# Kernel optimization log

Measured on AMD Instinct MI355X. Metric: run time of the kernel, lower is better.

Reference implementation:

```python
import jax, jax.numpy as jnp
import numpy as np

B, S, V, E, H, NL, DFF = 16, 16, 64, 64, 8, 4, 2048
L = S * V
DH = E // H
NUM_GRIDS = 100
POI_DIM = 8
OV_DIM = 8


def setup_inputs() -> dict:
    key = jax.random.key(0)
    ks = jax.random.split(key, 32)
    sc = 0.05
    inp = {}
    inp['features'] = jax.random.normal(ks[0], (B, S, V, 3), jnp.float32)
    inp['overlap_tag'] = jax.random.randint(ks[1], (B, S, V), 0, 3)
    inp['poi_id'] = jax.random.randint(ks[2], (B, S, V), 0, NUM_GRIDS + 1)
    # embedders
    inp['W_raw'] = jax.random.normal(ks[3], (3, E), jnp.float32) * sc
    inp['b_raw'] = jnp.zeros((E,), jnp.float32)
    inp['pos_tab'] = jax.random.normal(ks[4], (S, E), jnp.float32) * sc
    inp['type_tab'] = jax.random.normal(ks[5], (V, E), jnp.float32) * sc
    inp['poi_tab'] = jax.random.normal(ks[6], (NUM_GRIDS + 1, POI_DIM), jnp.float32) * sc
    inp['overlap_tab'] = jax.random.normal(ks[7], (3, OV_DIM), jnp.float32) * sc
    inp['W_comb'] = jax.random.normal(ks[8], (E + OV_DIM + POI_DIM, E), jnp.float32) * sc
    inp['b_comb'] = jnp.zeros((E,), jnp.float32)
    # transformer layers (stacked over NL)
    inp['Wqkv'] = jax.random.normal(ks[9], (NL, E, 3 * E), jnp.float32) * sc
    inp['bqkv'] = jnp.zeros((NL, 3 * E), jnp.float32)
    inp['Wo'] = jax.random.normal(ks[10], (NL, E, E), jnp.float32) * sc
    inp['bo'] = jnp.zeros((NL, E), jnp.float32)
    inp['ln1_s'] = jnp.ones((NL, E), jnp.float32)
    inp['ln1_b'] = jnp.zeros((NL, E), jnp.float32)
    inp['W1'] = jax.random.normal(ks[11], (NL, E, DFF), jnp.float32) * sc
    inp['b1'] = jnp.zeros((NL, DFF), jnp.float32)
    inp['W2'] = jax.random.normal(ks[12], (NL, DFF, E), jnp.float32) * sc
    inp['b2'] = jnp.zeros((NL, E), jnp.float32)
    inp['ln2_s'] = jnp.ones((NL, E), jnp.float32)
    inp['ln2_b'] = jnp.zeros((NL, E), jnp.float32)
    inp['W_head'] = jax.random.normal(ks[13], (E, 3), jnp.float32) * sc
    inp['b_head'] = jnp.zeros((3,), jnp.float32)
    return inp


def _layer_norm(x, s, b):
    m = x.mean(-1, keepdims=True)
    v = ((x - m) ** 2).mean(-1, keepdims=True)
    return (x - m) / jnp.sqrt(v + 1e-5) * s + b


def _forward(features, overlap_tag, poi_id, W_raw, b_raw, pos_tab, type_tab,
             poi_tab, overlap_tab, W_comb, b_comb, Wqkv, bqkv, Wo, bo,
             ln1_s, ln1_b, W1, b1, W2, b2, ln2_s, ln2_b, W_head, b_head):
    # padding_idx=0 rows are zero (as in nn.Embedding(padding_idx=0))
    poi_tab = poi_tab.at[0].set(0.0)
    overlap_tab = overlap_tab.at[0].set(0.0)

    zero_mask = (features.sum(-1) == 0).reshape(B, L)  # [B, L]
    ov_idx = jnp.maximum(overlap_tag, 0)
    poi_idx = jnp.maximum(poi_id, 0)

    feat_e = features @ W_raw + b_raw                    # [B,S,V,E]
    concat = jnp.concatenate([feat_e, overlap_tab[ov_idx], poi_tab[poi_idx]], axis=-1)
    x = (concat @ W_comb + b_comb).reshape(B, L, E)      # [B,L,E]

    t_idx = jnp.repeat(jnp.arange(S), V)                 # [L]
    v_idx = jnp.tile(jnp.arange(V), S)                   # [L]
    struct_mask = (t_idx[:, None] != t_idx[None, :]) & (v_idx[:, None] != v_idx[None, :])
    full_mask = struct_mask[None] | zero_mask[:, None, :] | zero_mask[:, :, None]  # [B,L,L]
    bias = jnp.where(full_mask, -jnp.inf, 0.0)[:, None, :, :]  # [B,1,L,L]

    x = x + pos_tab[t_idx][None] + type_tab[v_idx][None]

    scale = 1.0 / jnp.sqrt(jnp.asarray(DH, x.dtype))
    for l in range(NL):
        qkv = x @ Wqkv[l] + bqkv[l]                      # [B,L,3E]
        q, k, v = jnp.split(qkv, 3, axis=-1)
        q = q.reshape(B, L, H, DH)
        k = k.reshape(B, L, H, DH)
        v = v.reshape(B, L, H, DH)
        scores = jnp.einsum('bqhd,bkhd->bhqk', q, k) * scale + bias
        attn = jax.nn.softmax(scores, axis=-1)
        o = jnp.einsum('bhqk,bkhd->bqhd', attn, v).reshape(B, L, E)
        x = _layer_norm(x + o @ Wo[l] + bo[l], ln1_s[l], ln1_b[l])
        ff = jax.nn.relu(x @ W1[l] + b1[l]) @ W2[l] + b2[l]
        x = _layer_norm(x + ff, ln2_s[l], ln2_b[l])

    last = x.reshape(B, S, V, E)[:, -1]                  # [B,V,E]
    return last @ W_head + b_head                        # [B,V,3]


def reference(features, overlap_tag, poi_id, W_raw, b_raw, pos_tab, type_tab,
              poi_tab, overlap_tab, W_comb, b_comb, Wqkv, bqkv, Wo, bo,
              ln1_s, ln1_b, W1, b1, W2, b2, ln2_s, ln2_b, W_head, b_head):
    return _forward(features, overlap_tag, poi_id, W_raw, b_raw, pos_tab, type_tab,
                    poi_tab, overlap_tab, W_comb, b_comb, Wqkv, bqkv, Wo, bo,
                    ln1_s, ln1_b, W1, b1, W2, b2, ln2_s, ln2_b, W_head, b_head)
```

## Files before the change

kernel.cpp:

```cpp
#include <hip/hip_runtime.h>
#include <math.h>

#define BB 16
#define SS 16
#define VVV 64
#define EE 64
#define HHH 8
#define NLAYER 4
#define DFF_ 2048
#define LL 1024
#define BL 16384
#define PERL 131072

typedef __attribute__((ext_vector_type(8))) _Float16 half8;
typedef __attribute__((ext_vector_type(4))) _Float16 half4v;
typedef __attribute__((ext_vector_type(2))) _Float16 half2v;
typedef __attribute__((ext_vector_type(4))) float f32x4;

#if defined(__has_builtin)
#if __has_builtin(__builtin_amdgcn_fdot2)
#define HAVE_FDOT2 1
#endif
#endif

#define SW64(m, k)  (((m) << 6) + ((((k) >> 3) ^ ((m) & 7)) << 3) + ((k) & 7))


__global__ __launch_bounds__(256) void k_prep(
    const float* __restrict__ W1, const float* __restrict__ W2,
    const float* __restrict__ Wqkv, const float* __restrict__ Wo,
    const float* __restrict__ Wcomb,
    _Float16* __restrict__ w1f, _Float16* __restrict__ w2f,
    _Float16* __restrict__ wqkvf, _Float16* __restrict__ wof,
    _Float16* __restrict__ wcombt)
{
  __shared__ float t[64 * 65];
  int bx = blockIdx.x;
  int cc = threadIdx.x & 63, rr = threadIdx.x >> 6;

  if (bx >= 272) {
    int r0 = (bx - 272) * 64;
#pragma unroll
    for (int i = 0; i < 16; i++) {
      int r = i * 4 + rr;
      if (r0 + r < 80) t[r * 65 + cc] = Wcomb[(size_t)(r0 + r) * 64 + cc];
    }
    __syncthreads();
#pragma unroll
    for (int i = 0; i < 16; i++) {
      int c = i * 4 + rr;
      if (r0 + c < 80) wcombt[(size_t)cc * 80 + r0 + c] = (_Float16)t[c * 65 + cc];
    }
    return;
  }

  const float* src; _Float16* dst; int astr;
  if (bx < 128) {
    int l = bx >> 5, g = bx & 31;
    src = W1 + (size_t)l * PERL + g * 64; astr = 2048;
    dst = w1f + (size_t)(l * 32 + g) * 4096;
  } else if (bx < 256) {
    int j = bx - 128; int l = j >> 5, g = j & 31;
    src = W2 + (size_t)l * PERL + (size_t)g * 64 * 64; astr = 64;
    dst = w2f + (size_t)(l * 32 + g) * 4096;
  } else if (bx < 268) {
    int j = bx - 256; int l = j / 3, g = j % 3;
    src = Wqkv + (size_t)l * 64 * 192 + g * 64; astr = 192;
    dst = wqkvf + (size_t)(l * 3 + g) * 4096;
  } else {
    int l = bx - 268;
    src = Wo + (size_t)l * 4096; astr = 64;
    dst = wof + (size_t)l * 4096;
  }
#pragma unroll
  for (int i = 0; i < 16; i++) {
    int a = i * 4 + rr;
    t[cc * 65 + a] = src[(size_t)a * astr + cc];
  }
  __syncthreads();
#pragma unroll
  for (int it = 0; it < 2; it++) {
    int c = threadIdx.x + it * 256;
    int frag = c >> 6, lane = c & 63;
    int m = (frag >> 1) * 16 + (lane & 15);
    int k0 = (frag & 1) * 32 + (lane >> 4) * 8;
    const float* tr = &t[m * 65 + k0];
    half8 h;
#pragma unroll
    for (int j = 0; j < 8; j++) h[j] = (_Float16)tr[j];
    *(half8*)&dst[(size_t)c * 8] = h;
  }
}

__device__ __forceinline__ void qkv_nb(
    const half8 (&af)[2][2], const _Float16* __restrict__ wqkvf,
    const float* __restrict__ bqkv, _Float16* __restrict__ qbuf,
    _Float16* __restrict__ kbuf, _Float16* __restrict__ vbuf,
    int bx, int nb, int wm, int wn, int lane)
{
  int quad = lane >> 4, l15 = lane & 15;
  const _Float16* bt = wqkvf + (size_t)nb * 4096;
  half8 bf[2][2];
#pragma unroll
  for (int nt = 0; nt < 2; nt++)
#pragma unroll
    for (int ks = 0; ks < 2; ks++)
      bf[nt][ks] = *(const half8*)&bt[(size_t)(((wn * 2 + nt) * 2 + ks) * 512) +
                                      lane * 8];
  f32x4 acc[2][2];
#pragma unroll
  for (int mt = 0; mt < 2; mt++)
#pragma unroll
    for (int nt = 0; nt < 2; nt++) {
      float bv = bqkv[nb * 64 + wn * 32 + nt * 16 + l15];
      acc[mt][nt] = (f32x4){bv, bv, bv, bv};
    }
#pragma unroll
  for (int ks = 0; ks < 2; ks++)
#pragma unroll
    for (int mt = 0; mt < 2; mt++)
#pragma unroll
      for (int nt = 0; nt < 2; nt++)
        acc[mt][nt] = __builtin_amdgcn_mfma_f32_16x16x32_f16(
            af[mt][ks], bf[nt][ks], acc[mt][nt], 0, 0, 0);
  _Float16* dst = (nb == 0) ? qbuf : ((nb == 1) ? kbuf : vbuf);
#pragma unroll
  for (int mt = 0; mt < 2; mt++)
#pragma unroll
    for (int nt = 0; nt < 2; nt++) {
      int col = wn * 32 + nt * 16 + l15;
      int h = col >> 3, d = col & 7;
#pragma unroll
      for (int r = 0; r < 4; r++) {
        int row = bx * 64 + wm * 32 + mt * 16 + quad * 4 + r;
        int b = row >> 10, rb = row & 1023;
        dst[((size_t)(b * 8 + h) * 1024 + rb) * 8 + d] = (_Float16)acc[mt][nt][r];
      }
    }
}

__device__ __forceinline__ void ffn_load(
    const _Float16* __restrict__ w1f, const _Float16* __restrict__ w2f, int g,
    half8 (&a1)[2][2], half8 (&b2w)[2][2], int wm, int wn, int lane)
{
  const _Float16* w1t_ = w1f + (size_t)g * 4096;
  const _Float16* w2t_ = w2f + (size_t)g * 4096;
#pragma unroll
  for (int ht = 0; ht < 2; ht++)
#pragma unroll
    for (int ks = 0; ks < 2; ks++)
      a1[ht][ks] = *(const half8*)&w1t_[(size_t)(((wm * 2 + ht) * 2 + ks) * 512) +
                                        lane * 8];
#pragma unroll
  for (int nt = 0; nt < 2; nt++)
#pragma unroll
    for (int ks = 0; ks < 2; ks++)
      b2w[nt][ks] = *(const half8*)&w2t_[(size_t)(((wn * 2 + nt) * 2 + ks) * 512) +
                                         lane * 8];
}

__device__ __forceinline__ void ffn_step(
    const half8 (&a1)[2][2], const half8 (&b2w)[2][2], const half8 (&xb)[2][2],
    _Float16* hsbuf, const float* __restrict__ b1, int g, f32x4 (&acc)[2][2],
    int wm, int wn, int lane)
{
  int quad = lane >> 4, l15 = lane & 15;
  f32x4 hacc[2][2];
#pragma unroll
  for (int ht = 0; ht < 2; ht++)
#pragma unroll
    for (int mt = 0; mt < 2; mt++) hacc[ht][mt] = (f32x4){0.f, 0.f, 0.f, 0.f};
#pragma unroll
  for (int ks = 0; ks < 2; ks++)
#pragma unroll
    for (int ht = 0; ht < 2; ht++)
#pragma unroll
      for (int mt = 0; mt < 2; mt++)
        hacc[ht][mt] = __builtin_amdgcn_mfma_f32_16x16x32_f16(
            a1[ht][ks], xb[mt][ks], hacc[ht][mt], 0, 0, 0);
#pragma unroll
  for (int ht = 0; ht < 2; ht++) {
    float4 bb = *(const float4*)&b1[g * 64 + wm * 32 + ht * 16 + quad * 4];
#pragma unroll
    for (int mt = 0; mt < 2; mt++) {
      f32x4 hv = hacc[ht][mt];
      half4v hp = (half4v){
          (_Float16)fmaxf(hv[0] + bb.x, 0.f), (_Float16)fmaxf(hv[1] + bb.y, 0.f),
          (_Float16)fmaxf(hv[2] + bb.z, 0.f), (_Float16)fmaxf(hv[3] + bb.w, 0.f)};
      *(half4v*)&hsbuf[SW64(wn * 32 + mt * 16 + l15,
                            wm * 32 + ht * 16 + quad * 4)] = hp;
    }
  }
  __syncthreads();
#pragma unroll
  for (int ks = 0; ks < 2; ks++)
#pragma unroll
    for (int mt = 0; mt < 2; mt++) {
      half8 a2 = *(const half8*)&hsbuf[SW64(wm * 32 + mt * 16 + l15,
                                            ks * 32 + quad * 8)];
#pragma unroll
      for (int nt = 0; nt < 2; nt++)
        acc[mt][nt] = __builtin_amdgcn_mfma_f32_16x16x32_f16(a2, b2w[nt][ks],
                                                             acc[mt][nt], 0, 0, 0);
    }
}

__global__ __launch_bounds__(256) void k_embqkv(
    const float* __restrict__ features, const int* __restrict__ ovtag,
    const int* __restrict__ poiid, const float* __restrict__ W_raw,
    const float* __restrict__ b_raw, const float* __restrict__ ov_tab,
    const float* __restrict__ poi_tab, const _Float16* __restrict__ wcombt,
    const float* __restrict__ b_comb, const float* __restrict__ pos_tab,
    const float* __restrict__ type_tab, float* __restrict__ x1,
    float* __restrict__ zm, const _Float16* __restrict__ wqkvf,
    const float* __restrict__ bqkv, _Float16* __restrict__ qbuf,
    _Float16* __restrict__ kbuf, _Float16* __restrict__ vbuf)
{
  constexpr int KP = 104;
  __shared__ _Float16 As[64 * KP];
  __shared__ _Float16 Bs[64 * KP];
  __shared__ _Float16 xs[4096];
  int tid = threadIdx.x;
  int bx = blockIdx.x;
  int m0 = bx * 64;
  int wave = tid >> 6, lane = tid & 63, quad = lane >> 4, l15 = lane & 15;
  int wm = wave >> 1, wn = wave & 1;
  for (int p = tid; p < 1536; p += 256) {
    int r = p / 24, s = p - r * 24; int c = s * 4;
    int row = m0 + r;
    float f0 = features[row * 3 + 0];
    float f1 = features[row * 3 + 1];
    float f2 = features[row * 3 + 2];
    if (s == 0) zm[row] = ((f0 + f1 + f2) == 0.f) ? 1.f : 0.f;
    half4v h;
#pragma unroll
    for (int j = 0; j < 4; j++) {
      int cc = c + j; float v;
      if (cc < 64) {
        v = b_raw[cc] + f0 * W_raw[cc] + f1 * W_raw[64 + cc] + f2 * W_raw[128 + cc];
      } else if (cc < 72) {
        int tt = ovtag[row]; v = (tt <= 0) ? 0.f : ov_tab[tt * 8 + cc - 64];
      } else if (cc < 80) {
        int tt = poiid[row]; v = (tt <= 0) ? 0.f : poi_tab[tt * 8 + cc - 72];
      } else v = 0.f;
      h[j] = (_Float16)v;
    }
    *(half4v*)&As[r * KP + c] = h;
  }
  for (int p = tid; p < 1536; p += 256) {
    int r = p / 24, s = p - r * 24; int c = s * 4;
    half4v h = (half4v){0, 0, 0, 0};
    if (c < 80) h = *(const half4v*)&wcombt[r * 80 + c];
    *(half4v*)&Bs[r * KP + c] = h;
  }
  __syncthreads();
  f32x4 acc[2][2];
#pragma unroll
  for (int mt = 0; mt < 2; mt++)
#pragma unroll
    for (int nt = 0; nt < 2; nt++) {
      float bv = b_comb[wn * 32 + nt * 16 + l15];
      acc[mt][nt] = (f32x4){bv, bv, bv, bv};
    }
#pragma unroll
  for (int ks = 0; ks < 3; ks++) {
    half8 af[2], bf[2];
#pragma unroll
    for (int mt = 0; mt < 2; mt++)
      af[mt] = *(const half8*)&As[(wm * 32 + mt * 16 + l15) * KP + ks * 32 + quad * 8];
#pragma unroll
    for (int nt = 0; nt < 2; nt++)
      bf[nt] = *(const half8*)&Bs[(wn * 32 + nt * 16 + l15) * KP + ks * 32 + quad * 8];
#pragma unroll
    for (int mt = 0; mt < 2; mt++)
#pragma unroll
      for (int nt = 0; nt < 2; nt++)
        acc[mt][nt] = __builtin_amdgcn_mfma_f32_16x16x32_f16(af[mt], bf[nt],
                                                             acc[mt][nt], 0, 0, 0);
  }
#pragma unroll
  for (int mt = 0; mt < 2; mt++)
#pragma unroll
    for (int nt = 0; nt < 2; nt++)
#pragma unroll
      for (int r = 0; r < 4; r++) {
        int lrow = wm * 32 + mt * 16 + quad * 4 + r;
        int row = m0 + lrow;
        int col = wn * 32 + nt * 16 + l15;
        int l = row & (LL - 1);
        float v = acc[mt][nt][r] +
            pos_tab[(l >> 6) * 64 + col] + type_tab[(l & 63) * 64 + col];
        x1[(size_t)row * 64 + col] = v;
        xs[SW64(lrow, col)] = (_Float16)v;
      }
  __syncthreads();
  half8 af[2][2];
#pragma unroll
  for (int mt = 0; mt < 2; mt++)
#pragma unroll
    for (int ks = 0; ks < 2; ks++)
      af[mt][ks] = *(const half8*)&xs[SW64(wm * 32 + mt * 16 + l15,
                                           ks * 32 + quad * 8)];
  for (int nb = 0; nb < 3; nb++)
    qkv_nb(af, wqkvf, bqkv, qbuf, kbuf, vbuf, bx, nb, wm, wn, lane);
}

__global__ __launch_bounds__(256) void k_attn2(
    const _Float16* __restrict__ qbuf, const _Float16* __restrict__ kbuf,
    const _Float16* __restrict__ vbuf, const float* __restrict__ zm,
    _Float16* __restrict__ obuf)
{
  __shared__ _Float16 Ks[1024 * 8];
  __shared__ _Float16 Vs[1024 * 8];
  __shared__ float zs[1024];
  int blk = blockIdx.x;
  int qb = blk & 3, h = (blk >> 2) & 7, b = blk >> 5;
  int qrow = qb * 256 + threadIdx.x;
  half8 qh = *(const half8*)&qbuf[(size_t)(b * 8 + h) * 8192 + (size_t)qrow * 8];
  const _Float16* kb = kbuf + (size_t)(b * 8 + h) * 8192;
  const _Float16* vb = vbuf + (size_t)(b * 8 + h) * 8192;
  for (int p = threadIdx.x; p < 1024; p += 256) {
    *(half8*)&Ks[p * 8] = *(const half8*)&kb[p * 8];
    *(half8*)&Vs[p * 8] = *(const half8*)&vb[p * 8];
    zs[p] = zm[b * LL + p];
  }
  __syncthreads();
  int tq = qrow >> 6, vq = qrow & 63;
  const float scale = 0.3535533905932738f;
  float m = -INFINITY, lsum = 0.f;
  float acc[8] = {0.f, 0.f, 0.f, 0.f, 0.f, 0.f, 0.f, 0.f};
  bool zmq = (zs[qrow] != 0.f);

  auto attend = [&](int k) {
    if (zs[k] != 0.f) return;
    half8 kk = *(const half8*)&Ks[k * 8];
    float s = 0.f;
#ifdef HAVE_FDOT2
#pragma unroll
    for (int j = 0; j < 4; j++) {
      half2v qa = (half2v){qh[2 * j], qh[2 * j + 1]};
      half2v ka = (half2v){kk[2 * j], kk[2 * j + 1]};
      s = __builtin_amdgcn_fdot2(qa, ka, s, false);
    }
#else
#pragma unroll
    for (int j = 0; j < 8; j++) s += (float)qh[j] * (float)kk[j];
#endif
    s *= scale;
    half8 vv = *(const half8*)&Vs[k * 8];
    if (s <= m) {
      float p = __expf(s - m);
      lsum += p;
#pragma unroll
      for (int d = 0; d < 8; d++) acc[d] += p * (float)vv[d];
    } else {
      float r = __expf(m - s);
      lsum = lsum * r + 1.f;
#pragma unroll
      for (int d = 0; d < 8; d++) acc[d] = acc[d] * r + (float)vv[d];
      m = s;
    }
  };

  if (!zmq) {
    for (int vv = 0; vv < 64; vv++) attend(tq * 64 + vv);
    for (int tt = 0; tt < 16; tt++) {
      if (tt == tq) continue;
      attend(tt * 64 + vq);
    }
  }
  float inv = 1.f / lsum;
  half8 o;
#pragma unroll
  for (int d = 0; d < 8; d++) o[d] = (_Float16)(acc[d] * inv);
  size_t tile = (size_t)(b * 16 + (qrow >> 6));
  int frag = ((qrow >> 4) & 3) * 2 + (h >> 2);
  int flane = (h & 3) * 16 + (qrow & 15);
  *(half8*)&obuf[tile * 4096 + frag * 512 + flane * 8] = o;
}

__global__ __launch_bounds__(512) void k_layer(
    const _Float16* __restrict__ obuf, const _Float16* __restrict__ wof,
    const float* __restrict__ bo, float* __restrict__ x1,
    const float* __restrict__ ln1_s, const float* __restrict__ ln1_b,
    const _Float16* __restrict__ w1f, const _Float16* __restrict__ w2f,
    const float* __restrict__ b1, const float* __restrict__ b2,
    const float* __restrict__ ln2_s, const float* __restrict__ ln2_b,
    const _Float16* __restrict__ wqkvf, const float* __restrict__ bqkv,
    _Float16* __restrict__ qbuf, _Float16* __restrict__ kbuf,
    _Float16* __restrict__ vbuf, int doqkv,
    const float* __restrict__ Wh, const float* __restrict__ bh,
    float* __restrict__ out)
{
  __shared__ float ots[64 * 68];
  __shared__ _Float16 xs[4096];
  __shared__ float x2f[4096];
  __shared__ _Float16 hs[2][2][4096];
  int tid = threadIdx.x;
  int bx = blockIdx.x;
  int wave = tid >> 6, lane = tid & 63;
  int quad = lane >> 4, l15 = lane & 15;
  int grp = wave >> 2, w4 = wave & 3;
  int wm = w4 >> 1, wn = w4 & 1;

  {
    const _Float16* ot = obuf + (size_t)bx * 4096;
    int mq = grp * 2 + wm;
    half8 af[2], bf[2][2];
#pragma unroll
    for (int ks = 0; ks < 2; ks++)
      af[ks] = *(const half8*)&ot[(size_t)((mq * 2 + ks) * 512) + lane * 8];
#pragma unroll
    for (int nt = 0; nt < 2; nt++)
#pragma unroll
      for (int ks = 0; ks < 2; ks++)
        bf[nt][ks] = *(const half8*)&wof[(size_t)(((wn * 2 + nt) * 2 + ks) * 512) +
                                         lane * 8];
    f32x4 acc[2];
#pragma unroll
    for (int nt = 0; nt < 2; nt++) {
      float bv = bo[wn * 32 + nt * 16 + l15];
      acc[nt] = (f32x4){bv, bv, bv, bv};
    }
#pragma unroll
    for (int ks = 0; ks < 2; ks++)
#pragma unroll
      for (int nt = 0; nt < 2; nt++)
        acc[nt] = __builtin_amdgcn_mfma_f32_16x16x32_f16(af[ks], bf[nt][ks],
                                                         acc[nt], 0, 0, 0);
#pragma unroll
    for (int nt = 0; nt < 2; nt++)
#pragma unroll
      for (int r = 0; r < 4; r++)
        ots[(mq * 16 + quad * 4 + r) * 68 + wn * 32 + nt * 16 + l15] = acc[nt][r];
  }
  __syncthreads();
  for (int i = 0; i < 8; i++) {
    int row = wave * 8 + i;
    size_t off = (size_t)(bx * 64 + row) * 64 + lane;
    float val = ots[row * 68 + lane] + x1[off];
    float sum = val;
#pragma unroll
    for (int o = 32; o > 0; o >>= 1) sum += __shfl_xor(sum, o);
    float mean = sum * (1.f / 64.f);
    float d = val - mean;
    float sq = d * d;
#pragma unroll
    for (int o = 32; o > 0; o >>= 1) sq += __shfl_xor(sq, o);
    float xv = d * rsqrtf(sq * (1.f / 64.f) + 1e-5f) * ln1_s[lane] + ln1_b[lane];
    x2f[row * 64 + lane] = xv;
    xs[SW64(row, lane)] = (_Float16)xv;
  }
  __syncthreads();

  half8 xb[2][2];
#pragma unroll
  for (int mt = 0; mt < 2; mt++)
#pragma unroll
    for (int ks = 0; ks < 2; ks++)
      xb[mt][ks] = *(const half8*)&xs[SW64(wn * 32 + mt * 16 + l15,
                                           ks * 32 + quad * 8)];
  f32x4 acc[2][2];
#pragma unroll
  for (int mt = 0; mt < 2; mt++)
#pragma unroll
    for (int nt = 0; nt < 2; nt++) {
      float bv = (grp == 0) ? b2[wn * 32 + nt * 16 + l15] : 0.f;
      acc[mt][nt] = (f32x4){bv, bv, bv, bv};
    }
  half8 a1x[2][2], b2x[2][2], a1y[2][2], b2y[2][2];
  ffn_load(w1f, w2f, grp, a1x, b2x, wm, wn, lane);
  for (int ii = 0; ii < 8; ii++) {
    ffn_load(w1f, w2f, ii * 4 + 2 + grp, a1y, b2y, wm, wn, lane);
    ffn_step(a1x, b2x, xb, &hs[grp][0][0], b1, ii * 4 + grp, acc, wm, wn, lane);
    if (ii < 7) ffn_load(w1f, w2f, ii * 4 + 4 + grp, a1x, b2x, wm, wn, lane);
    ffn_step(a1y, b2y, xb, &hs[grp][1][0], b1, ii * 4 + 2 + grp, acc, wm, wn, lane);
  }
  __syncthreads();
  if (grp == 0) {
#pragma unroll
    for (int mt = 0; mt < 2; mt++)
#pragma unroll
      for (int nt = 0; nt < 2; nt++)
#pragma unroll
        for (int r = 0; r < 4; r++)
          ots[(wm * 32 + mt * 16 + quad * 4 + r) * 68 + wn * 32 + nt * 16 + l15] =
              acc[mt][nt][r];
  }
  __syncthreads();
  if (grp == 1) {
#pragma unroll
    for (int mt = 0; mt < 2; mt++)
#pragma unroll
      for (int nt = 0; nt < 2; nt++)
#pragma unroll
        for (int r = 0; r < 4; r++)
          ots[(wm * 32 + mt * 16 + quad * 4 + r) * 68 + wn * 32 + nt * 16 + l15] +=
              acc[mt][nt][r];
  }
  __syncthreads();
  for (int i = 0; i < 8; i++) {
    int row = wave * 8 + i;
    size_t off = (size_t)(bx * 64 + row) * 64 + lane;
    float val = ots[row * 68 + lane] + x2f[row * 64 + lane];
    float sum = val;
#pragma unroll
    for (int o = 32; o > 0; o >>= 1) sum += __shfl_xor(sum, o);
    float mean = sum * (1.f / 64.f);
    float d = val - mean;
    float sq = d * d;
#pragma unroll
    for (int o = 32; o > 0; o >>= 1) sq += __shfl_xor(sq, o);
    float xv = d * rsqrtf(sq * (1.f / 64.f) + 1e-5f) * ln2_s[lane] + ln2_b[lane];
    x1[off] = xv;
    x2f[row * 64 + lane] = xv;
    xs[SW64(row, lane)] = (_Float16)xv;
  }
  if (!doqkv) {
    __syncthreads();
    if ((bx & 15) == 15 && tid < 192) {
      int b = bx >> 4;
      int v = tid / 3, j = tid - v * 3;
      float a = bh[j];
      for (int e = 0; e < 64; e++)
        a += x2f[v * 64 + e] * Wh[e * 3 + j];
      out[((size_t)(b * 64 + v)) * 3 + j] = a;
    }
    return;
  }
  __syncthreads();
  half8 af[2][2];
#pragma unroll
  for (int mt = 0; mt < 2; mt++)
#pragma unroll
    for (int ks = 0; ks < 2; ks++)
      af[mt][ks] = *(const half8*)&xs[SW64(wm * 32 + mt * 16 + l15,
                                           ks * 32 + quad * 8)];
  for (int nb = grp; nb < 3; nb += 2)
    qkv_nb(af, wqkvf, bqkv, qbuf, kbuf, vbuf, bx, nb, wm, wn, lane);
}

extern "C" void kernel_launch(void* const* d_in, const int* in_sizes, int n_in,
                              void* d_out, int out_size, void* d_ws, size_t ws_size,
                              hipStream_t stream) {
  const float* features = (const float*)d_in[0];
  const int*   ovtag    = (const int*)d_in[1];
  const int*   poiid    = (const int*)d_in[2];
  const float* W_raw    = (const float*)d_in[3];
  const float* b_raw    = (const float*)d_in[4];
  const float* pos_tab  = (const float*)d_in[5];
  const float* type_tab = (const float*)d_in[6];
  const float* poi_tab  = (const float*)d_in[7];
  const float* ov_tab   = (const float*)d_in[8];
  const float* W_comb   = (const float*)d_in[9];
  const float* b_comb   = (const float*)d_in[10];
  const float* Wqkv     = (const float*)d_in[11];
  const float* bqkv     = (const float*)d_in[12];
  const float* Wo       = (const float*)d_in[13];
  const float* bo       = (const float*)d_in[14];
  const float* ln1_s    = (const float*)d_in[15];
  const float* ln1_b    = (const float*)d_in[16];
  const float* W1       = (const float*)d_in[17];
  const float* b1       = (const float*)d_in[18];
  const float* W2       = (const float*)d_in[19];
  const float* b2       = (const float*)d_in[20];
  const float* ln2_s    = (const float*)d_in[21];
  const float* ln2_b    = (const float*)d_in[22];
  const float* W_head   = (const float*)d_in[23];
  const float* b_head   = (const float*)d_in[24];
  float* out = (float*)d_out;
  float* ws  = (float*)d_ws;

  float* zm  = ws;
  float* x1  = zm + BL;
  _Float16* qbuf   = (_Float16*)(x1 + (size_t)BL * 64);
  _Float16* kbuf   = qbuf + (size_t)BL * 64;
  _Float16* vbuf   = kbuf + (size_t)BL * 64;
  _Float16* obuf16 = vbuf + (size_t)BL * 64;
  _Float16* wcombt = obuf16 + (size_t)BL * 64;
  _Float16* w1f    = wcombt + 5120;
  _Float16* w2f    = w1f + (size_t)NLAYER * PERL;
  _Float16* wqkvf  = w2f + (size_t)NLAYER * PERL;
  _Float16* wof    = wqkvf + (size_t)NLAYER * 3 * 4096;

  k_prep<<<274, 256, 0, stream>>>(W1, W2, Wqkv, Wo, W_comb,
                                  w1f, w2f, wqkvf, wof, wcombt);
  k_embqkv<<<256, 256, 0, stream>>>(features, ovtag, poiid, W_raw, b_raw,
                                    ov_tab, poi_tab, wcombt, b_comb,
                                    pos_tab, type_tab, x1, zm,
                                    wqkvf, bqkv, qbuf, kbuf, vbuf);
  for (int l = 0; l < NLAYER; l++) {
    k_attn2<<<512, 256, 0, stream>>>(qbuf, kbuf, vbuf, zm, obuf16);
    int doqkv = (l < NLAYER - 1);
    k_layer<<<256, 512, 0, stream>>>(
        obuf16, wof + (size_t)l * 4096, bo + l * EE, x1,
        ln1_s + l * EE, ln1_b + l * EE,
        w1f + (size_t)l * PERL, w2f + (size_t)l * PERL,
        b1 + l * DFF_, b2 + l * EE,
        ln2_s + l * EE, ln2_b + l * EE,
        wqkvf + (size_t)(l + 1 < NLAYER ? l + 1 : 0) * 3 * 4096,
        bqkv + (l + 1 < NLAYER ? l + 1 : 0) * 192,
        qbuf, kbuf, vbuf, doqkv, W_head, b_head, out);
  }
}
```

Before: 317.4 us.

## Fuse embedding and all transformer layers into one persistent cooperative kernel

Replaces the per-layer attention and layer kernels with a single cooperative kernel of 256 blocks that keeps each block's 64-token activation tile resident in LDS across all layers, using grid.sync between layers. Only K/V go through global memory, double-buffered by layer parity. Q and the attention output stay in LDS, and FFN weights are staged through a triple-buffered LDS ring. This removes kernel launch gaps and the global round trips for x, q and o, at the cost of grid-wide barriers, heavy LDS use and less parallelism in attention, since there is now one block per 64 tokens.

```diff
diff --git a/kernel.cpp b/kernel.cpp
--- a/kernel.cpp
+++ b/kernel.cpp
@@ -1,5 +1,8 @@
 #include <hip/hip_runtime.h>
+#include <hip/hip_cooperative_groups.h>
 #include <math.h>
+
+namespace cg = cooperative_groups;
 
 #define BB 16
 #define SS 16
@@ -92,452 +95,377 @@
   }
 }
 
-__device__ __forceinline__ void qkv_nb(
-    const half8 (&af)[2][2], const _Float16* __restrict__ wqkvf,
-    const float* __restrict__ bqkv, _Float16* __restrict__ qbuf,
-    _Float16* __restrict__ kbuf, _Float16* __restrict__ vbuf,
-    int bx, int nb, int wm, int wn, int lane)
+struct NetParams {
+  const float* features; const int* ovtag; const int* poiid;
+  const float* W_raw; const float* b_raw;
+  const float* ov_tab; const float* poi_tab;
+  const _Float16* wcombt; const float* b_comb;
+  const float* pos_tab; const float* type_tab;
+  float* zm;
+  const _Float16* wqkvf; const float* bqkv;
+  const _Float16* wof;   const float* bo;
+  const _Float16* w1f;   const _Float16* w2f;
+  const float* b1; const float* b2;
+  const float* ln1_s; const float* ln1_b;
+  const float* ln2_s; const float* ln2_b;
+  _Float16* kv;
+  const float* Wh; const float* bh; float* out;
+};
+
+__global__ __launch_bounds__(512) void k_net(NetParams P)
 {
+  cg::grid_group grid = cg::this_grid();
+  __shared__ float    xf[4096];
+  __shared__ _Float16 xs[4096];
+  __shared__ _Float16 qlds[4096];
+  __shared__ float    ots[64 * 68];
+  __shared__ float    zs[1024];
+  __shared__ _Float16 wlds[3][8192];
+  __shared__ _Float16 hs[2][4096];
+
+  int tid = threadIdx.x, bx = blockIdx.x;
+  int wave = tid >> 6, lane = tid & 63;
   int quad = lane >> 4, l15 = lane & 15;
-  const _Float16* bt = wqkvf + (size_t)nb * 4096;
-  half8 bf[2][2];
-#pragma unroll
-  for (int nt = 0; nt < 2; nt++)
-#pragma unroll
-    for (int ks = 0; ks < 2; ks++)
-      bf[nt][ks] = *(const half8*)&bt[(size_t)(((wn * 2 + nt) * 2 + ks) * 512) +
-                                      lane * 8];
-  f32x4 acc[2][2];
-#pragma unroll
-  for (int mt = 0; mt < 2; mt++)
+  int b = bx >> 4;
+
+  {
+    constexpr int KP = 104;
+    _Float16* As = &wlds[0][0];
+    _Float16* Bs = &wlds[0][0] + 64 * KP;
+    int m0 = bx * 64;
+    for (int p = tid; p < 1536; p += 512) {
+      int r = p / 24, s = p - r * 24; int c = s * 4;
+      int row = m0 + r;
+      float f0 = P.features[row * 3 + 0];
+      float f1 = P.features[row * 3 + 1];
+      float f2 = P.features[row * 3 + 2];
+      if (s == 0) P.zm[row] = ((f0 + f1 + f2) == 0.f) ? 1.f : 0.f;
+      half4v h;
+#pragma unroll
+      for (int j = 0; j < 4; j++) {
+        int cc = c + j; float v;
+        if (cc < 64) {
+          v = P.b_raw[cc] + f0 * P.W_raw[cc] + f1 * P.W_raw[64 + cc] +
+              f2 * P.W_raw[128 + cc];
+        } else if (cc < 72) {
+          int tt = P.ovtag[row]; v = (tt <= 0) ? 0.f : P.ov_tab[tt * 8 + cc - 64];
+        } else if (cc < 80) {
+          int tt = P.poiid[row]; v = (tt <= 0) ? 0.f : P.poi_tab[tt * 8 + cc - 72];
+        } else v = 0.f;
+        h[j] = (_Float16)v;
+      }
+      *(half4v*)&As[r * KP + c] = h;
+    }
+    for (int p = tid; p < 1536; p += 512) {
+      int r = p / 24, s = p - r * 24; int c = s * 4;
+      half4v h = (half4v){0, 0, 0, 0};
+      if (c < 80) h = *(const half4v*)&P.wcombt[r * 80 + c];
+      *(half4v*)&Bs[r * KP + c] = h;
+    }
+    __syncthreads();
+    int wm = wave >> 1, wn = wave & 1;
+    f32x4 acc[2];
 #pragma unroll
     for (int nt = 0; nt < 2; nt++) {
-      float bv = bqkv[nb * 64 + wn * 32 + nt * 16 + l15];
-      acc[mt][nt] = (f32x4){bv, bv, bv, bv};
-    }
-#pragma unroll
-  for (int ks = 0; ks < 2; ks++)
-#pragma unroll
-    for (int mt = 0; mt < 2; mt++)
-#pragma unroll
-      for (int nt = 0; nt < 2; nt++)
-        acc[mt][nt] = __builtin_amdgcn_mfma_f32_16x16x32_f16(
-            af[mt][ks], bf[nt][ks], acc[mt][nt], 0, 0, 0);
-  _Float16* dst = (nb == 0) ? qbuf : ((nb == 1) ? kbuf : vbuf);
-#pragma unroll
-  for (int mt = 0; mt < 2; mt++)
-#pragma unroll
-    for (int nt = 0; nt < 2; nt++) {
-      int col = wn * 32 + nt * 16 + l15;
-      int h = col >> 3, d = col & 7;
+      float bv = P.b_comb[wn * 32 + nt * 16 + l15];
+      acc[nt] = (f32x4){bv, bv, bv, bv};
+    }
+#pragma unroll
+    for (int ks = 0; ks < 3; ks++) {
+      half8 af = *(const half8*)&As[(wm * 16 + l15) * KP + ks * 32 + quad * 8];
+#pragma unroll
+      for (int nt = 0; nt < 2; nt++) {
+        half8 bf = *(const half8*)&Bs[(wn * 32 + nt * 16 + l15) * KP +
+                                      ks * 32 + quad * 8];
+        acc[nt] = __builtin_amdgcn_mfma_f32_16x16x32_f16(af, bf, acc[nt], 0, 0, 0);
+      }
+    }
+#pragma unroll
+    for (int nt = 0; nt < 2; nt++)
 #pragma unroll
       for (int r = 0; r < 4; r++) {
-        int row = bx * 64 + wm * 32 + mt * 16 + quad * 4 + r;
-        int b = row >> 10, rb = row & 1023;
-        dst[((size_t)(b * 8 + h) * 1024 + rb) * 8 + d] = (_Float16)acc[mt][nt][r];
-      }
-    }
-}
-
-__device__ __forceinline__ void ffn_load(
-    const _Float16* __restrict__ w1f, const _Float16* __restrict__ w2f, int g,
-    half8 (&a1)[2][2], half8 (&b2w)[2][2], int wm, int wn, int lane)
-{
-  const _Float16* w1t_ = w1f + (size_t)g * 4096;
-  const _Float16* w2t_ = w2f + (size_t)g * 4096;
-#pragma unroll
-  for (int ht = 0; ht < 2; ht++)
-#pragma unroll
-    for (int ks = 0; ks < 2; ks++)
-      a1[ht][ks] = *(const half8*)&w1t_[(size_t)(((wm * 2 + ht) * 2 + ks) * 512) +
-                                        lane * 8];
-#pragma unroll
-  for (int nt = 0; nt < 2; nt++)
-#pragma unroll
-    for (int ks = 0; ks < 2; ks++)
-      b2w[nt][ks] = *(const half8*)&w2t_[(size_t)(((wn * 2 + nt) * 2 + ks) * 512) +
-                                         lane * 8];
-}
-
-__device__ __forceinline__ void ffn_step(
-    const half8 (&a1)[2][2], const half8 (&b2w)[2][2], const half8 (&xb)[2][2],
-    _Float16* hsbuf, const float* __restrict__ b1, int g, f32x4 (&acc)[2][2],
-    int wm, int wn, int lane)
-{
-  int quad = lane >> 4, l15 = lane & 15;
-  f32x4 hacc[2][2];
-#pragma unroll
-  for (int ht = 0; ht < 2; ht++)
-#pragma unroll
-    for (int mt = 0; mt < 2; mt++) hacc[ht][mt] = (f32x4){0.f, 0.f, 0.f, 0.f};
-#pragma unroll
-  for (int ks = 0; ks < 2; ks++)
-#pragma unroll
-    for (int ht = 0; ht < 2; ht++)
-#pragma unroll
-      for (int mt = 0; mt < 2; mt++)
-        hacc[ht][mt] = __builtin_amdgcn_mfma_f32_16x16x32_f16(
-            a1[ht][ks], xb[mt][ks], hacc[ht][mt], 0, 0, 0);
-#pragma unroll
-  for (int ht = 0; ht < 2; ht++) {
-    float4 bb = *(const float4*)&b1[g * 64 + wm * 32 + ht * 16 + quad * 4];
-#pragma unroll
-    for (int mt = 0; mt < 2; mt++) {
-      f32x4 hv = hacc[ht][mt];
-      half4v hp = (half4v){
-          (_Float16)fmaxf(hv[0] + bb.x, 0.f), (_Float16)fmaxf(hv[1] + bb.y, 0.f),
-          (_Float16)fmaxf(hv[2] + bb.z, 0.f), (_Float16)fmaxf(hv[3] + bb.w, 0.f)};
-      *(half4v*)&hsbuf[SW64(wn * 32 + mt * 16 + l15,
-                            wm * 32 + ht * 16 + quad * 4)] = hp;
-    }
+        int lrow = wm * 16 + quad * 4 + r;
+        int col = wn * 32 + nt * 16 + l15;
+        int l = (m0 + lrow) & (LL - 1);
+        float v = acc[nt][r] + P.pos_tab[(l >> 6) * 64 + col] +
+                  P.type_tab[(l & 63) * 64 + col];
+        xf[lrow * 64 + col] = v;
+        xs[SW64(lrow, col)] = (_Float16)v;
+      }
   }
   __syncthreads();
-#pragma unroll
-  for (int ks = 0; ks < 2; ks++)
-#pragma unroll
-    for (int mt = 0; mt < 2; mt++) {
-      half8 a2 = *(const half8*)&hsbuf[SW64(wm * 32 + mt * 16 + l15,
-                                            ks * 32 + quad * 8)];
+
+  auto qkv_all = [&](const _Float16* wq, const float* bq, int set) {
+    int grp = wave >> 2, w4 = wave & 3;
+    int wm = w4 >> 1, wn = w4 & 1;
+    half8 af[2][2];
+#pragma unroll
+    for (int mt = 0; mt < 2; mt++)
+#pragma unroll
+      for (int ks = 0; ks < 2; ks++)
+        af[mt][ks] = *(const half8*)&xs[SW64(wm * 32 + mt * 16 + l15,
+                                             ks * 32 + quad * 8)];
+    for (int nb = grp; nb < 3; nb += 2) {
+      const _Float16* bt = wq + (size_t)nb * 4096;
+      half8 bf[2][2];
 #pragma unroll
       for (int nt = 0; nt < 2; nt++)
-        acc[mt][nt] = __builtin_amdgcn_mfma_f32_16x16x32_f16(a2, b2w[nt][ks],
-                                                             acc[mt][nt], 0, 0, 0);
-    }
-}
-
-__global__ __launch_bounds__(256) void k_embqkv(
-    const float* __restrict__ features, const int* __restrict__ ovtag,
-    const int* __restrict__ poiid, const float* __restrict__ W_raw,
-    const float* __restrict__ b_raw, const float* __restrict__ ov_tab,
-    const float* __restrict__ poi_tab, const _Float16* __restrict__ wcombt,
-    const float* __restrict__ b_comb, const float* __restrict__ pos_tab,
-    const float* __restrict__ type_tab, float* __restrict__ x1,
-    float* __restrict__ zm, const _Float16* __restrict__ wqkvf,
-    const float* __restrict__ bqkv, _Float16* __restrict__ qbuf,
-    _Float16* __restrict__ kbuf, _Float16* __restrict__ vbuf)
-{
-  constexpr int KP = 104;
-  __shared__ _Float16 As[64 * KP];
-  __shared__ _Float16 Bs[64 * KP];
-  __shared__ _Float16 xs[4096];
-  int tid = threadIdx.x;
-  int bx = blockIdx.x;
-  int m0 = bx * 64;
-  int wave = tid >> 6, lane = tid & 63, quad = lane >> 4, l15 = lane & 15;
-  int wm = wave >> 1, wn = wave & 1;
-  for (int p = tid; p < 1536; p += 256) {
-    int r = p / 24, s = p - r * 24; int c = s * 4;
-    int row = m0 + r;
-    float f0 = features[row * 3 + 0];
-    float f1 = features[row * 3 + 1];
-    float f2 = features[row * 3 + 2];
-    if (s == 0) zm[row] = ((f0 + f1 + f2) == 0.f) ? 1.f : 0.f;
-    half4v h;
-#pragma unroll
-    for (int j = 0; j < 4; j++) {
-      int cc = c + j; float v;
-      if (cc < 64) {
-        v = b_raw[cc] + f0 * W_raw[cc] + f1 * W_raw[64 + cc] + f2 * W_raw[128 + cc];
-      } else if (cc < 72) {
-        int tt = ovtag[row]; v = (tt <= 0) ? 0.f : ov_tab[tt * 8 + cc - 64];
-      } else if (cc < 80) {
-        int tt = poiid[row]; v = (tt <= 0) ? 0.f : poi_tab[tt * 8 + cc - 72];
-      } else v = 0.f;
-      h[j] = (_Float16)v;
-    }
-    *(half4v*)&As[r * KP + c] = h;
+#pragma unroll
+        for (int ks = 0; ks < 2; ks++)
+          bf[nt][ks] = *(const half8*)&bt[(size_t)(((wn * 2 + nt) * 2 + ks) * 512) +
+                                          lane * 8];
+      f32x4 acc[2][2];
+#pragma unroll
+      for (int mt = 0; mt < 2; mt++)
+#pragma unroll
+        for (int nt = 0; nt < 2; nt++) {
+          float bv = bq[nb * 64 + wn * 32 + nt * 16 + l15];
+          acc[mt][nt] = (f32x4){bv, bv, bv, bv};
+        }
+#pragma unroll
+      for (int ks = 0; ks < 2; ks++)
+#pragma unroll
+        for (int mt = 0; mt < 2; mt++)
+#pragma unroll
+          for (int nt = 0; nt < 2; nt++)
+            acc[mt][nt] = __builtin_amdgcn_mfma_f32_16x16x32_f16(
+                af[mt][ks], bf[nt][ks], acc[mt][nt], 0, 0, 0);
+#pragma unroll
+      for (int mt = 0; mt < 2; mt++)
+#pragma unroll
+        for (int nt = 0; nt < 2; nt++) {
+          int col = wn * 32 + nt * 16 + l15;
+          int h = col >> 3, d = col & 7;
+#pragma unroll
+          for (int r = 0; r < 4; r++) {
+            int m = wm * 32 + mt * 16 + quad * 4 + r;
+            _Float16 v = (_Float16)acc[mt][nt][r];
+            if (nb == 0) {
+              int frag = (m >> 4) * 2 + (h >> 2);
+              int fl = (h & 3) * 16 + (m & 15);
+              qlds[frag * 512 + fl * 8 + d] = v;
+            } else {
+              int which = nb - 1;
+              int rb = (bx & 15) * 64 + m;
+              P.kv[((size_t)((set * 2 + which) * (BB * 8) + b * 8 + h)) * 8192 +
+                   rb * 8 + d] = v;
+            }
+          }
+        }
+    }
+  };
+  qkv_all(P.wqkvf, P.bqkv, 0);
+
+  const float scale = 0.3535533905932738f;
+  for (int l = 0; l < NLAYER; l++) {
+    grid.sync();
+    if (l == 0) {
+      for (int p = tid; p < 1024; p += 512) zs[p] = P.zm[b * LL + p];
+      __syncthreads();
+    }
+    {
+      int h = wave;
+      int frag = (lane >> 4) * 2 + (h >> 2);
+      int fl = (h & 3) * 16 + (lane & 15);
+      half8 qh = *(const half8*)&qlds[frag * 512 + fl * 8];
+      const _Float16* kb = P.kv + ((size_t)(((l & 1) * 2 + 0) * (BB * 8) +
+                                            b * 8 + h)) * 8192;
+      const _Float16* vb = P.kv + ((size_t)(((l & 1) * 2 + 1) * (BB * 8) +
+                                            b * 8 + h)) * 8192;
+      int tqu = bx & 15;
+      int vq = lane;
+      float m = -INFINITY, lsum = 0.f;
+      float acc[8] = {0.f, 0.f, 0.f, 0.f, 0.f, 0.f, 0.f, 0.f};
+      bool zmq = (zs[tqu * 64 + lane] != 0.f);
+      auto attend = [&](int k) {
+        if (zs[k] != 0.f) return;
+        half8 kk = *(const half8*)&kb[k * 8];
+        float s = 0.f;
+#ifdef HAVE_FDOT2
+#pragma unroll
+        for (int j = 0; j < 4; j++) {
+          half2v qa = (half2v){qh[2 * j], qh[2 * j + 1]};
+          half2v ka = (half2v){kk[2 * j], kk[2 * j + 1]};
+          s = __builtin_amdgcn_fdot2(qa, ka, s, false);
+        }
+#else
+#pragma unroll
+        for (int j = 0; j < 8; j++) s += (float)qh[j] * (float)kk[j];
+#endif
+        s *= scale;
+        half8 vv = *(const half8*)&vb[k * 8];
+        float nm = fmaxf(m, s);
+        float rr = __expf(m - nm);
+        float p = __expf(s - nm);
+        lsum = lsum * rr + p;
+#pragma unroll
+        for (int d = 0; d < 8; d++) acc[d] = acc[d] * rr + p * (float)vv[d];
+        m = nm;
+      };
+      if (!zmq) {
+        for (int vv = 0; vv < 64; vv++) attend(tqu * 64 + vv);
+        for (int tt = 0; tt < 16; tt++) {
+          if (tt == tqu) continue;
+          attend(tt * 64 + vq);
+        }
+      }
+      float inv = 1.f / lsum;
+      half8 o;
+#pragma unroll
+      for (int d = 0; d < 8; d++) o[d] = (_Float16)(acc[d] * inv);
+      *(half8*)&qlds[frag * 512 + fl * 8] = o;
+    }
+    __syncthreads();
+    {
+      const _Float16* wof_l = P.wof + (size_t)l * 4096;
+      const float* bo_l = P.bo + l * EE;
+      int wm = wave >> 1, wn = wave & 1;
+      f32x4 acc[2];
+#pragma unroll
+      for (int nt = 0; nt < 2; nt++) {
+        float bv = bo_l[wn * 32 + nt * 16 + l15];
+        acc[nt] = (f32x4){bv, bv, bv, bv};
+      }
+#pragma unroll
+      for (int ks = 0; ks < 2; ks++) {
+        half8 af = *(const half8*)&qlds[(wm * 2 + ks) * 512 + lane * 8];
+#pragma unroll
+        for (int nt = 0; nt < 2; nt++) {
+          half8 bf = *(const half8*)&wof_l[(size_t)(((wn * 2 + nt) * 2 + ks) * 512) +
+                                           lane * 8];
+          acc[nt] = __builtin_amdgcn_mfma_f32_16x16x32_f16(af, bf, acc[nt], 0, 0, 0);
+        }
+      }
+#pragma unroll
+      for (int nt = 0; nt < 2; nt++)
+#pragma unroll
+        for (int r = 0; r < 4; r++)
+          ots[(wm * 16 + quad * 4 + r) * 68 + wn * 32 + nt * 16 + l15] = acc[nt][r];
+    }
+    __syncthreads();
+    {
+      const float* s1 = P.ln1_s + l * EE; const float* b1_ = P.ln1_b + l * EE;
+      for (int i = 0; i < 8; i++) {
+        int row = wave * 8 + i;
+        float val = ots[row * 68 + lane] + xf[row * 64 + lane];
+        float sum = val;
+#pragma unroll
+        for (int o = 32; o > 0; o >>= 1) sum += __shfl_xor(sum, o);
+        float mean = sum * (1.f / 64.f);
+        float d = val - mean;
+        float sq = d * d;
+#pragma unroll
+        for (int o = 32; o > 0; o >>= 1) sq += __shfl_xor(sq, o);
+        float xv = d * rsqrtf(sq * (1.f / 64.f) + 1e-5f) * s1[lane] + b1_[lane];
+        xf[row * 64 + lane] = xv;
+        xs[SW64(row, lane)] = (_Float16)xv;
+      }
+    }
+    __syncthreads();
+    {
+      const _Float16* w1l = P.w1f + (size_t)l * PERL;
+      const _Float16* w2l = P.w2f + (size_t)l * PERL;
+      const float* b1l = P.b1 + l * DFF_;
+      const float* b2l = P.b2 + l * EE;
+      int wh = wave >> 1, wm1 = wave & 1;
+      int wm2 = wave >> 1, wn2 = wave & 1;
+      half8 xb[2][2];
+#pragma unroll
+      for (int mt = 0; mt < 2; mt++)
+#pragma unroll
+        for (int ks = 0; ks < 2; ks++)
+          xb[mt][ks] = *(const half8*)&xs[SW64(wm1 * 32 + mt * 16 + l15,
+                                               ks * 32 + quad * 8)];
+      f32x4 acc[2];
+#pragma unroll
+      for (int nt = 0; nt < 2; nt++) {
+        float bv = b2l[wn2 * 32 + nt * 16 + l15];
+        acc[nt] = (f32x4){bv, bv, bv, bv};
+      }
+      *(half8*)&wlds[0][tid * 8] = *(const half8*)&w1l[tid * 8];
+      *(half8*)&wlds[0][4096 + tid * 8] = *(const half8*)&w2l[tid * 8];
+      __syncthreads();
+      for (int c = 0; c < 32; c++) {
+        int slot = c % 3, nslot = (c + 1) % 3;
+        f32x4 hacc[2] = {(f32x4){0.f, 0.f, 0.f, 0.f}, (f32x4){0.f, 0.f, 0.f, 0.f}};
+#pragma unroll
+        for (int ks = 0; ks < 2; ks++) {
+          half8 a1 = *(const half8*)&wlds[slot][(wh * 2 + ks) * 512 + lane * 8];
+#pragma unroll
+          for (int mt = 0; mt < 2; mt++)
+            hacc[mt] = __builtin_amdgcn_mfma_f32_16x16x32_f16(a1, xb[mt][ks],
+                                                              hacc[mt], 0, 0, 0);
+        }
+        float4 bb = *(const float4*)&b1l[c * 64 + wh * 16 + quad * 4];
+#pragma unroll
+        for (int mt = 0; mt < 2; mt++) {
+          f32x4 hv = hacc[mt];
+          half4v hp = (half4v){
+              (_Float16)fmaxf(hv[0] + bb.x, 0.f), (_Float16)fmaxf(hv[1] + bb.y, 0.f),
+              (_Float16)fmaxf(hv[2] + bb.z, 0.f), (_Float16)fmaxf(hv[3] + bb.w, 0.f)};
+          *(half4v*)&hs[c & 1][SW64(wm1 * 32 + mt * 16 + l15,
+                                    wh * 16 + quad * 4)] = hp;
+        }
+        if (c < 31) {
+          *(half8*)&wlds[nslot][tid * 8] =
+              *(const half8*)&w1l[(size_t)(c + 1) * 4096 + tid * 8];
+          *(half8*)&wlds[nslot][4096 + tid * 8] =
+              *(const half8*)&w2l[(size_t)(c + 1) * 4096 + tid * 8];
+        }
+        __syncthreads();
+#pragma unroll
+        for (int ks = 0; ks < 2; ks++) {
+          half8 a2 = *(const half8*)&hs[c & 1][SW64(wm2 * 16 + l15,
+                                                    ks * 32 + quad * 8)];
+#pragma unroll
+          for (int nt = 0; nt < 2; nt++) {
+            half8 b2w = *(const half8*)&wlds[slot][4096 +
+                ((wn2 * 2 + nt) * 2 + ks) * 512 + lane * 8];
+            acc[nt] = __builtin_amdgcn_mfma_f32_16x16x32_f16(a2, b2w, acc[nt],
+                                                             0, 0, 0);
+          }
+        }
+      }
+      __syncthreads();
+#pragma unroll
+      for (int nt = 0; nt < 2; nt++)
+#pragma unroll
+        for (int r = 0; r < 4; r++)
+          ots[(wm2 * 16 + quad * 4 + r) * 68 + wn2 * 32 + nt * 16 + l15] =
+              acc[nt][r];
+    }
+    __syncthreads();
+    {
+      const float* s2 = P.ln2_s + l * EE; const float* b2_ = P.ln2_b + l * EE;
+      for (int i = 0; i < 8; i++) {
+        int row = wave * 8 + i;
+        float val = ots[row * 68 + lane] + xf[row * 64 + lane];
+        float sum = val;
+#pragma unroll
+        for (int o = 32; o > 0; o >>= 1) sum += __shfl_xor(sum, o);
+        float mean = sum * (1.f / 64.f);
+        float d = val - mean;
+        float sq = d * d;
+#pragma unroll
+        for (int o = 32; o > 0; o >>= 1) sq += __shfl_xor(sq, o);
+        float xv = d * rsqrtf(sq * (1.f / 64.f) + 1e-5f) * s2[lane] + b2_[lane];
+        xf[row * 64 + lane] = xv;
+        xs[SW64(row, lane)] = (_Float16)xv;
+      }
+    }
+    __syncthreads();
+    if (l < NLAYER - 1) {
+      qkv_all(P.wqkvf + (size_t)(l + 1) * 3 * 4096, P.bqkv + (l + 1) * 192,
+              (l + 1) & 1);
+    } else {
+      if ((bx & 15) == 15 && tid < 192) {
+        int v = tid / 3, j = tid - v * 3;
+        float a = P.bh[j];
+        for (int e = 0; e < 64; e++) a += xf[v * 64 + e] * P.Wh[e * 3 + j];
+        P.out[((size_t)(b * 64 + v)) * 3 + j] = a;
+      }
+    }
   }
-  for (int p = tid; p < 1536; p += 256) {
-    int r = p / 24, s = p - r * 24; int c = s * 4;
-    half4v h = (half4v){0, 0, 0, 0};
-    if (c < 80) h = *(const half4v*)&wcombt[r * 80 + c];
-    *(half4v*)&Bs[r * KP + c] = h;
-  }
-  __syncthreads();
-  f32x4 acc[2][2];
-#pragma unroll
-  for (int mt = 0; mt < 2; mt++)
-#pragma unroll
-    for (int nt = 0; nt < 2; nt++) {
-      float bv = b_comb[wn * 32 + nt * 16 + l15];
-      acc[mt][nt] = (f32x4){bv, bv, bv, bv};
-    }
-#pragma unroll
-  for (int ks = 0; ks < 3; ks++) {
-    half8 af[2], bf[2];
-#pragma unroll
-    for (int mt = 0; mt < 2; mt++)
-      af[mt] = *(const half8*)&As[(wm * 32 + mt * 16 + l15) * KP + ks * 32 + quad * 8];
-#pragma unroll
-    for (int nt = 0; nt < 2; nt++)
-      bf[nt] = *(const half8*)&Bs[(wn * 32 + nt * 16 + l15) * KP + ks * 32 + quad * 8];
-#pragma unroll
-    for (int mt = 0; mt < 2; mt++)
-#pragma unroll
-      for (int nt = 0; nt < 2; nt++)
-        acc[mt][nt] = __builtin_amdgcn_mfma_f32_16x16x32_f16(af[mt], bf[nt],
-                                                             acc[mt][nt], 0, 0, 0);
-  }
-#pragma unroll
-  for (int mt = 0; mt < 2; mt++)
-#pragma unroll
-    for (int nt = 0; nt < 2; nt++)
-#pragma unroll
-      for (int r = 0; r < 4; r++) {
-        int lrow = wm * 32 + mt * 16 + quad * 4 + r;
-        int row = m0 + lrow;
-        int col = wn * 32 + nt * 16 + l15;
-        int l = row & (LL - 1);
-        float v = acc[mt][nt][r] +
-            pos_tab[(l >> 6) * 64 + col] + type_tab[(l & 63) * 64 + col];
-        x1[(size_t)row * 64 + col] = v;
-        xs[SW64(lrow, col)] = (_Float16)v;
-      }
-  __syncthreads();
-  half8 af[2][2];
-#pragma unroll
-  for (int mt = 0; mt < 2; mt++)
-#pragma unroll
-    for (int ks = 0; ks < 2; ks++)
-      af[mt][ks] = *(const half8*)&xs[SW64(wm * 32 + mt * 16 + l15,
-                                           ks * 32 + quad * 8)];
-  for (int nb = 0; nb < 3; nb++)
-    qkv_nb(af, wqkvf, bqkv, qbuf, kbuf, vbuf, bx, nb, wm, wn, lane);
-}
-
-__global__ __launch_bounds__(256) void k_attn2(
-    const _Float16* __restrict__ qbuf, const _Float16* __restrict__ kbuf,
-    const _Float16* __restrict__ vbuf, const float* __restrict__ zm,
-    _Float16* __restrict__ obuf)
-{
-  __shared__ _Float16 Ks[1024 * 8];
-  __shared__ _Float16 Vs[1024 * 8];
-  __shared__ float zs[1024];
-  int blk = blockIdx.x;
-  int qb = blk & 3, h = (blk >> 2) & 7, b = blk >> 5;
-  int qrow = qb * 256 + threadIdx.x;
-  half8 qh = *(const half8*)&qbuf[(size_t)(b * 8 + h) * 8192 + (size_t)qrow * 8];
-  const _Float16* kb = kbuf + (size_t)(b * 8 + h) * 8192;
-  const _Float16* vb = vbuf + (size_t)(b * 8 + h) * 8192;
-  for (int p = threadIdx.x; p < 1024; p += 256) {
-    *(half8*)&Ks[p * 8] = *(const half8*)&kb[p * 8];
-    *(half8*)&Vs[p * 8] = *(const half8*)&vb[p * 8];
-    zs[p] = zm[b * LL + p];
-  }
-  __syncthreads();
-  int tq = qrow >> 6, vq = qrow & 63;
-  const float scale = 0.3535533905932738f;
-  float m = -INFINITY, lsum = 0.f;
-  float acc[8] = {0.f, 0.f, 0.f, 0.f, 0.f, 0.f, 0.f, 0.f};
-  bool zmq = (zs[qrow] != 0.f);
-
-  auto attend = [&](int k) {
-    if (zs[k] != 0.f) return;
-    half8 kk = *(const half8*)&Ks[k * 8];
-    float s = 0.f;
-#ifdef HAVE_FDOT2
-#pragma unroll
-    for (int j = 0; j < 4; j++) {
-      half2v qa = (half2v){qh[2 * j], qh[2 * j + 1]};
-      half2v ka = (half2v){kk[2 * j], kk[2 * j + 1]};
-      s = __builtin_amdgcn_fdot2(qa, ka, s, false);
-    }
-#else
-#pragma unroll
-    for (int j = 0; j < 8; j++) s += (float)qh[j] * (float)kk[j];
-#endif
-    s *= scale;
-    half8 vv = *(const half8*)&Vs[k * 8];
-    if (s <= m) {
-      float p = __expf(s - m);
-      lsum += p;
-#pragma unroll
-      for (int d = 0; d < 8; d++) acc[d] += p * (float)vv[d];
-    } else {
-      float r = __expf(m - s);
-      lsum = lsum * r + 1.f;
-#pragma unroll
-      for (int d = 0; d < 8; d++) acc[d] = acc[d] * r + (float)vv[d];
-      m = s;
-    }
-  };
-
-  if (!zmq) {
-    for (int vv = 0; vv < 64; vv++) attend(tq * 64 + vv);
-    for (int tt = 0; tt < 16; tt++) {
-      if (tt == tq) continue;
-      attend(tt * 64 + vq);
-    }
-  }
-  float inv = 1.f / lsum;
-  half8 o;
-#pragma unroll
-  for (int d = 0; d < 8; d++) o[d] = (_Float16)(acc[d] * inv);
-  size_t tile = (size_t)(b * 16 + (qrow >> 6));
-  int frag = ((qrow >> 4) & 3) * 2 + (h >> 2);
-  int flane = (h & 3) * 16 + (qrow & 15);
-  *(half8*)&obuf[tile * 4096 + frag * 512 + flane * 8] = o;
-}
-
-__global__ __launch_bounds__(512) void k_layer(
-    const _Float16* __restrict__ obuf, const _Float16* __restrict__ wof,
-    const float* __restrict__ bo, float* __restrict__ x1,
-    const float* __restrict__ ln1_s, const float* __restrict__ ln1_b,
-    const _Float16* __restrict__ w1f, const _Float16* __restrict__ w2f,
-    const float* __restrict__ b1, const float* __restrict__ b2,
-    const float* __restrict__ ln2_s, const float* __restrict__ ln2_b,
-    const _Float16* __restrict__ wqkvf, const float* __restrict__ bqkv,
-    _Float16* __restrict__ qbuf, _Float16* __restrict__ kbuf,
-    _Float16* __restrict__ vbuf, int doqkv,
-    const float* __restrict__ Wh, const float* __restrict__ bh,
-    float* __restrict__ out)
-{
-  __shared__ float ots[64 * 68];
-  __shared__ _Float16 xs[4096];
-  __shared__ float x2f[4096];
-  __shared__ _Float16 hs[2][2][4096];
-  int tid = threadIdx.x;
-  int bx = blockIdx.x;
-  int wave = tid >> 6, lane = tid & 63;
-  int quad = lane >> 4, l15 = lane & 15;
-  int grp = wave >> 2, w4 = wave & 3;
-  int wm = w4 >> 1, wn = w4 & 1;
-
-  {
-    const _Float16* ot = obuf + (size_t)bx * 4096;
-    int mq = grp * 2 + wm;
-    half8 af[2], bf[2][2];
-#pragma unroll
-    for (int ks = 0; ks < 2; ks++)
-      af[ks] = *(const half8*)&ot[(size_t)((mq * 2 + ks) * 512) + lane * 8];
-#pragma unroll
-    for (int nt = 0; nt < 2; nt++)
-#pragma unroll
-      for (int ks = 0; ks < 2; ks++)
-        bf[nt][ks] = *(const half8*)&wof[(size_t)(((wn * 2 + nt) * 2 + ks) * 512) +
-                                         lane * 8];
-    f32x4 acc[2];
-#pragma unroll
-    for (int nt = 0; nt < 2; nt++) {
-      float bv = bo[wn * 32 + nt * 16 + l15];
-      acc[nt] = (f32x4){bv, bv, bv, bv};
-    }
-#pragma unroll
-    for (int ks = 0; ks < 2; ks++)
-#pragma unroll
-      for (int nt = 0; nt < 2; nt++)
-        acc[nt] = __builtin_amdgcn_mfma_f32_16x16x32_f16(af[ks], bf[nt][ks],
-                                                         acc[nt], 0, 0, 0);
-#pragma unroll
-    for (int nt = 0; nt < 2; nt++)
-#pragma unroll
-      for (int r = 0; r < 4; r++)
-        ots[(mq * 16 + quad * 4 + r) * 68 + wn * 32 + nt * 16 + l15] = acc[nt][r];
-  }
-  __syncthreads();
-  for (int i = 0; i < 8; i++) {
-    int row = wave * 8 + i;
-    size_t off = (size_t)(bx * 64 + row) * 64 + lane;
-    float val = ots[row * 68 + lane] + x1[off];
-    float sum = val;
-#pragma unroll
-    for (int o = 32; o > 0; o >>= 1) sum += __shfl_xor(sum, o);
-    float mean = sum * (1.f / 64.f);
-    float d = val - mean;
-    float sq = d * d;
-#pragma unroll
-    for (int o = 32; o > 0; o >>= 1) sq += __shfl_xor(sq, o);
-    float xv = d * rsqrtf(sq * (1.f / 64.f) + 1e-5f) * ln1_s[lane] + ln1_b[lane];
-    x2f[row * 64 + lane] = xv;
-    xs[SW64(row, lane)] = (_Float16)xv;
-  }
-  __syncthreads();
-
-  half8 xb[2][2];
-#pragma unroll
-  for (int mt = 0; mt < 2; mt++)
-#pragma unroll
-    for (int ks = 0; ks < 2; ks++)
-      xb[mt][ks] = *(const half8*)&xs[SW64(wn * 32 + mt * 16 + l15,
-                                           ks * 32 + quad * 8)];
-  f32x4 acc[2][2];
-#pragma unroll
-  for (int mt = 0; mt < 2; mt++)
-#pragma unroll
-    for (int nt = 0; nt < 2; nt++) {
-      float bv = (grp == 0) ? b2[wn * 32 + nt * 16 + l15] : 0.f;
-      acc[mt][nt] = (f32x4){bv, bv, bv, bv};
-    }
-  half8 a1x[2][2], b2x[2][2], a1y[2][2], b2y[2][2];
-  ffn_load(w1f, w2f, grp, a1x, b2x, wm, wn, lane);
-  for (int ii = 0; ii < 8; ii++) {
-    ffn_load(w1f, w2f, ii * 4 + 2 + grp, a1y, b2y, wm, wn, lane);
-    ffn_step(a1x, b2x, xb, &hs[grp][0][0], b1, ii * 4 + grp, acc, wm, wn, lane);
-    if (ii < 7) ffn_load(w1f, w2f, ii * 4 + 4 + grp, a1x, b2x, wm, wn, lane);
-    ffn_step(a1y, b2y, xb, &hs[grp][1][0], b1, ii * 4 + 2 + grp, acc, wm, wn, lane);
-  }
-  __syncthreads();
-  if (grp == 0) {
-#pragma unroll
-    for (int mt = 0; mt < 2; mt++)
-#pragma unroll
-      for (int nt = 0; nt < 2; nt++)
-#pragma unroll
-        for (int r = 0; r < 4; r++)
-          ots[(wm * 32 + mt * 16 + quad * 4 + r) * 68 + wn * 32 + nt * 16 + l15] =
-              acc[mt][nt][r];
-  }
-  __syncthreads();
-  if (grp == 1) {
-#pragma unroll
-    for (int mt = 0; mt < 2; mt++)
-#pragma unroll
-      for (int nt = 0; nt < 2; nt++)
-#pragma unroll
-        for (int r = 0; r < 4; r++)
-          ots[(wm * 32 + mt * 16 + quad * 4 + r) * 68 + wn * 32 + nt * 16 + l15] +=
-              acc[mt][nt][r];
-  }
-  __syncthreads();
-  for (int i = 0; i < 8; i++) {
-    int row = wave * 8 + i;
-    size_t off = (size_t)(bx * 64 + row) * 64 + lane;
-    float val = ots[row * 68 + lane] + x2f[row * 64 + lane];
-    float sum = val;
-#pragma unroll
-    for (int o = 32; o > 0; o >>= 1) sum += __shfl_xor(sum, o);
-    float mean = sum * (1.f / 64.f);
-    float d = val - mean;
-    float sq = d * d;
-#pragma unroll
-    for (int o = 32; o > 0; o >>= 1) sq += __shfl_xor(sq, o);
-    float xv = d * rsqrtf(sq * (1.f / 64.f) + 1e-5f) * ln2_s[lane] + ln2_b[lane];
-    x1[off] = xv;
-    x2f[row * 64 + lane] = xv;
-    xs[SW64(row, lane)] = (_Float16)xv;
-  }
-  if (!doqkv) {
-    __syncthreads();
-    if ((bx & 15) == 15 && tid < 192) {
-      int b = bx >> 4;
-      int v = tid / 3, j = tid - v * 3;
-      float a = bh[j];
-      for (int e = 0; e < 64; e++)
-        a += x2f[v * 64 + e] * Wh[e * 3 + j];
-      out[((size_t)(b * 64 + v)) * 3 + j] = a;
-    }
-    return;
-  }
-  __syncthreads();
-  half8 af[2][2];
-#pragma unroll
-  for (int mt = 0; mt < 2; mt++)
-#pragma unroll
-    for (int ks = 0; ks < 2; ks++)
-      af[mt][ks] = *(const half8*)&xs[SW64(wm * 32 + mt * 16 + l15,
-                                           ks * 32 + quad * 8)];
-  for (int nb = grp; nb < 3; nb += 2)
-    qkv_nb(af, wqkvf, bqkv, qbuf, kbuf, vbuf, bx, nb, wm, wn, lane);
 }
 
 extern "C" void kernel_launch(void* const* d_in, const int* in_sizes, int n_in,
@@ -571,13 +499,9 @@
   float* out = (float*)d_out;
   float* ws  = (float*)d_ws;
 
-  float* zm  = ws;
-  float* x1  = zm + BL;
-  _Float16* qbuf   = (_Float16*)(x1 + (size_t)BL * 64);
-  _Float16* kbuf   = qbuf + (size_t)BL * 64;
-  _Float16* vbuf   = kbuf + (size_t)BL * 64;
-  _Float16* obuf16 = vbuf + (size_t)BL * 64;
-  _Float16* wcombt = obuf16 + (size_t)BL * 64;
+  float* zm = ws;
+  _Float16* kv     = (_Float16*)(zm + BL);
+  _Float16* wcombt = kv + 4 * (size_t)BL * 64;
   _Float16* w1f    = wcombt + 5120;
   _Float16* w2f    = w1f + (size_t)NLAYER * PERL;
   _Float16* wqkvf  = w2f + (size_t)NLAYER * PERL;
@@ -585,21 +509,15 @@
 
   k_prep<<<274, 256, 0, stream>>>(W1, W2, Wqkv, Wo, W_comb,
                                   w1f, w2f, wqkvf, wof, wcombt);
-  k_embqkv<<<256, 256, 0, stream>>>(features, ovtag, poiid, W_raw, b_raw,
-                                    ov_tab, poi_tab, wcombt, b_comb,
-                                    pos_tab, type_tab, x1, zm,
-                                    wqkvf, bqkv, qbuf, kbuf, vbuf);
-  for (int l = 0; l < NLAYER; l++) {
-    k_attn2<<<512, 256, 0, stream>>>(qbuf, kbuf, vbuf, zm, obuf16);
-    int doqkv = (l < NLAYER - 1);
-    k_layer<<<256, 512, 0, stream>>>(
-        obuf16, wof + (size_t)l * 4096, bo + l * EE, x1,
-        ln1_s + l * EE, ln1_b + l * EE,
-        w1f + (size_t)l * PERL, w2f + (size_t)l * PERL,
-        b1 + l * DFF_, b2 + l * EE,
-        ln2_s + l * EE, ln2_b + l * EE,
-        wqkvf + (size_t)(l + 1 < NLAYER ? l + 1 : 0) * 3 * 4096,
-        bqkv + (l + 1 < NLAYER ? l + 1 : 0) * 192,
-        qbuf, kbuf, vbuf, doqkv, W_head, b_head, out);
-  }
+  NetParams p;
+  p.features = features; p.ovtag = ovtag; p.poiid = poiid;
+  p.W_raw = W_raw; p.b_raw = b_raw; p.ov_tab = ov_tab; p.poi_tab = poi_tab;
+  p.wcombt = wcombt; p.b_comb = b_comb; p.pos_tab = pos_tab; p.type_tab = type_tab;
+  p.zm = zm; p.wqkvf = wqkvf; p.bqkv = bqkv; p.wof = wof; p.bo = bo;
+  p.w1f = w1f; p.w2f = w2f; p.b1 = b1; p.b2 = b2;
+  p.ln1_s = ln1_s; p.ln1_b = ln1_b; p.ln2_s = ln2_s; p.ln2_b = ln2_b;
+  p.kv = kv; p.Wh = W_head; p.bh = b_head; p.out = out;
+  void* args[] = {&p};
+  hipLaunchCooperativeKernel((const void*)k_net, dim3(256), dim3(512), args, 0,
+                             stream);
 }
```

Result: slower. 488.3 us (+53.8%).
